# Kernel tuning notes

Measured on AMD Instinct MI355X. Metric: run time of the kernel, lower is better.

Reference implementation:

```python
import jax, jax.numpy as jnp
import numpy as np

N = 200000   # active voxels
K = 27       # 3^3 kernel offsets
C = 64       # feature channels (in == out -> residual is Identity)
EPS = 1e-5   # BatchNorm eps (torch default)


def setup_inputs() -> dict:
    key = jax.random.key(0)
    k0, k1, k2, k3 = jax.random.split(key, 4)
    x = jax.random.normal(k0, (N, C), dtype=jnp.float32)
    # neighbor map: for each output voxel and kernel offset, index of input voxel
    nbr_idx = jax.random.randint(k1, (N, K), 0, N, dtype=jnp.int64)
    W1 = jax.random.normal(k2, (K, C, C), dtype=jnp.float32) * 0.05
    W2 = jax.random.normal(k3, (K, C, C), dtype=jnp.float32) * 0.05
    gamma1 = jnp.ones((C,), jnp.float32)
    beta1 = jnp.zeros((C,), jnp.float32)
    gamma2 = jnp.ones((C,), jnp.float32)
    beta2 = jnp.zeros((C,), jnp.float32)
    return {"x": x, "nbr_idx": nbr_idx, "W1": W1, "gamma1": gamma1,
            "beta1": beta1, "W2": W2, "gamma2": gamma2, "beta2": beta2}


def batchnorm(x, gamma, beta):
    # train-mode BatchNorm1d over the voxel axis (biased variance)
    mu = x.mean(axis=0)
    var = x.var(axis=0)
    return (x - mu) * jax.lax.rsqrt(var + EPS) * gamma + beta


def sparse_conv(x, nbr_idx, W):
    # gather-GEMM-scatter sparse conv, streamed over the 27 kernel offsets
    # x: [N, Cin], nbr_idx: [N, K], W: [K, Cin, Cout]
    def body(acc, kw):
        idx, Wk = kw                      # idx: [N], Wk: [Cin, Cout]
        return acc + x[idx] @ Wk, None
    acc0 = jnp.zeros((x.shape[0], W.shape[2]), x.dtype)
    acc, _ = jax.lax.scan(body, acc0, (nbr_idx.T, W))
    return acc


def reference(x, nbr_idx, W1, gamma1, beta1, W2, gamma2, beta2):
    residual = x  # in_features == out_features -> Identity residual
    out = sparse_conv(jax.nn.relu(batchnorm(x, gamma1, beta1)), nbr_idx, W1)
    out = sparse_conv(jax.nn.relu(batchnorm(out, gamma2, beta2)), nbr_idx, W2)
    return out + residual
```

## Files before the change

kernel.cpp:

```cpp
#include <hip/hip_runtime.h>


#define KOFF 27

typedef __bf16 bf16x8 __attribute__((ext_vector_type(8)));
typedef float floatx4 __attribute__((ext_vector_type(4)));

__device__ __forceinline__ unsigned short f2bf(float x) {
    union { float f; unsigned int u; } v; v.f = x;
    unsigned int u = v.u;
    unsigned int r = u + 0x7FFFu + ((u >> 16) & 1u);
    return (unsigned short)(r >> 16);
}
__device__ __forceinline__ float bf2f(unsigned short s) {
    union { float f; unsigned int u; } v; v.u = ((unsigned int)s) << 16; return v.f;
}

__global__ void prep2(const float* __restrict__ W1, const float* __restrict__ W2,
                      unsigned short* __restrict__ W1f, unsigned short* __restrict__ W2f,
                      const float* __restrict__ x, float* __restrict__ stats,
                      int total4) {
    int b = blockIdx.x, t = threadIdx.x;
    if (b < 54) {
        __shared__ float sW[64 * 68];
        int k = b % 27;
        const float* src = (b < 27 ? W1 : W2) + k * 4096;
        unsigned short* dst = (b < 27 ? W1f : W2f) + (size_t)k * 4096;
        #pragma unroll
        for (int i = 0; i < 4; ++i) {
            int i4 = t + i * 256;
            float4 v = ((const float4*)src)[i4];
            int f = i4 * 4, r = f >> 6, c = f & 63;
            sW[r * 68 + c]     = v.x;
            sW[r * 68 + c + 1] = v.y;
            sW[r * 68 + c + 2] = v.z;
            sW[r * 68 + c + 3] = v.w;
        }
        __syncthreads();
        int fi = (t >> 5) & 7, ct = fi >> 1, ks = fi & 1;
        unsigned short o[16];
        #pragma unroll
        for (int d = 0; d < 2; ++d) {
            int lane2 = (t * 2 + d) & 63, q = lane2 >> 4, l15 = lane2 & 15;
            #pragma unroll
            for (int j = 0; j < 8; ++j) {
                int cin = ks * 32 + q * 8 + j, cout = ct * 16 + l15;
                o[d * 8 + j] = f2bf(sW[cin * 68 + cout]);
            }
        }
        ((uint4*)(dst + t * 16))[0] = *(const uint4*)(o);
        ((uint4*)(dst + t * 16))[1] = *(const uint4*)(o + 8);
        return;
    }
    __shared__ float s[128];
    if (t < 128) s[t] = 0.f;
    __syncthreads();
    int i = (b - 54) * 256 + t;
    int stride = (gridDim.x - 54) * 256;
    float a0 = 0.f, a1 = 0.f, a2 = 0.f, a3 = 0.f;
    float b0 = 0.f, b1 = 0.f, b2 = 0.f, b3 = 0.f;
    for (; i < total4; i += stride) {
        float4 v = ((const float4*)x)[i];
        a0 += v.x; b0 += v.x * v.x;
        a1 += v.y; b1 += v.y * v.y;
        a2 += v.z; b2 += v.z * v.z;
        a3 += v.w; b3 += v.w * v.w;
    }
    int c0 = (t << 2) & 63;
    atomicAdd(&s[c0],     a0); atomicAdd(&s[c0 + 1],     a1);
    atomicAdd(&s[c0 + 2], a2); atomicAdd(&s[c0 + 3],     a3);
    atomicAdd(&s[64 + c0],     b0); atomicAdd(&s[64 + c0 + 1], b1);
    atomicAdd(&s[64 + c0 + 2], b2); atomicAdd(&s[64 + c0 + 3], b3);
    __syncthreads();
    if (t < 64) { atomicAdd(&stats[t], s[t]); atomicAdd(&stats[64 + t], s[64 + t]); }
}

__global__ void bn_relu_f32(const float* __restrict__ in, const float* __restrict__ sums,
                            const float* __restrict__ gamma, const float* __restrict__ beta,
                            unsigned short* __restrict__ out, int total4, float invN) {
    __shared__ float sab[128];
    int t = threadIdx.x;
    if (t < 64) {
        float mu  = sums[t] * invN;
        float var = fmaxf(sums[64 + t] * invN - mu * mu, 0.f);
        float a   = gamma[t] * rsqrtf(var + 1e-5f);
        sab[t] = a; sab[64 + t] = beta[t] - mu * a;
    }
    __syncthreads();
    int i = blockIdx.x * blockDim.x + t;
    int stride = gridDim.x * blockDim.x;
    for (; i < total4; i += stride) {
        float4 v = ((const float4*)in)[i];
        int c0 = (i << 2) & 63;
        ushort4 o;
        o.x = f2bf(fmaxf(sab[c0]     * v.x + sab[64 + c0],     0.f));
        o.y = f2bf(fmaxf(sab[c0 + 1] * v.y + sab[64 + c0 + 1], 0.f));
        o.z = f2bf(fmaxf(sab[c0 + 2] * v.z + sab[64 + c0 + 2], 0.f));
        o.w = f2bf(fmaxf(sab[c0 + 3] * v.w + sab[64 + c0 + 3], 0.f));
        ((ushort4*)out)[i] = o;
    }
}

__global__ void bn_relu_b16(const unsigned short* __restrict__ in, const float* __restrict__ sums,
                            const float* __restrict__ gamma, const float* __restrict__ beta,
                            unsigned short* __restrict__ out, int total8, float invN) {
    __shared__ float sab[128];
    int t = threadIdx.x;
    if (t < 64) {
        float mu  = sums[t] * invN;
        float var = fmaxf(sums[64 + t] * invN - mu * mu, 0.f);
        float a   = gamma[t] * rsqrtf(var + 1e-5f);
        sab[t] = a; sab[64 + t] = beta[t] - mu * a;
    }
    __syncthreads();
    int i = blockIdx.x * blockDim.x + t;
    int stride = gridDim.x * blockDim.x;
    for (; i < total8; i += stride) {
        uint4 v = ((const uint4*)in)[i];
        int c0 = (i << 3) & 63;
        unsigned int w[4] = {v.x, v.y, v.z, v.w};
        unsigned int o[4];
        #pragma unroll
        for (int p = 0; p < 4; ++p) {
            float f0 = bf2f((unsigned short)(w[p] & 0xffff));
            float f1 = bf2f((unsigned short)(w[p] >> 16));
            int c = c0 + p * 2;
            unsigned short r0 = f2bf(fmaxf(sab[c]     * f0 + sab[64 + c],     0.f));
            unsigned short r1 = f2bf(fmaxf(sab[c + 1] * f1 + sab[64 + c + 1], 0.f));
            o[p] = (unsigned int)r0 | ((unsigned int)r1 << 16);
        }
        ((uint4*)out)[i] = make_uint4(o[0], o[1], o[2], o[3]);
    }
}

#define MFMA(a, b, c) __builtin_amdgcn_mfma_f32_16x16x32_bf16(a, b, c, 0, 0, 0)
#define WAIT_LGKM0() __builtin_amdgcn_s_waitcnt(0xC07F)

__global__ __launch_bounds__(256, 4) void spconv(
        const unsigned short* __restrict__ h,
        const int* __restrict__ idx,
        const unsigned short* __restrict__ Wf,
        unsigned short* __restrict__ outb,
        float* __restrict__ outf,
        const float* __restrict__ resid,
        float* __restrict__ stats,
        int N) {
    __shared__ float4 arena[1088];
    __shared__ float sred[128];
    unsigned short* sBb = (unsigned short*)arena;
    float* sE = (float*)arena;

    int t = threadIdx.x, lane = t & 63, wid = t >> 6;
    int q = lane >> 4, l15 = lane & 15;
    int base = blockIdx.x * 128;
    if (t < 128) sred[t] = 0.f;

    int r0 = base + wid * 32 + l15;
    int r1 = r0 + 16;
    const int* ip0 = idx + (size_t)min(r0, N - 1) * KOFF;
    const int* ip1 = idx + (size_t)min(r1, N - 1) * KOFF;
    int qo = q * 8;

    floatx4 acc[2][4];
    #pragma unroll
    for (int a_ = 0; a_ < 2; ++a_)
        #pragma unroll
        for (int b_ = 0; b_ < 4; ++b_)
            acc[a_][b_] = floatx4{0.f, 0.f, 0.f, 0.f};

    bf16x8 A0[4], A1[4], A2[4];
    {
        int g0 = ip0[0], g1 = ip1[0];
        const unsigned short* p0 = h + ((size_t)g0 << 6) + qo;
        const unsigned short* p1 = h + ((size_t)g1 << 6) + qo;
        A0[0] = *(const bf16x8*)p0; A0[1] = *(const bf16x8*)(p0 + 32);
        A0[2] = *(const bf16x8*)p1; A0[3] = *(const bf16x8*)(p1 + 32);
        g0 = ip0[1]; g1 = ip1[1];
        p0 = h + ((size_t)g0 << 6) + qo;
        p1 = h + ((size_t)g1 << 6) + qo;
        A1[0] = *(const bf16x8*)p0; A1[1] = *(const bf16x8*)(p0 + 32);
        A1[2] = *(const bf16x8*)p1; A1[3] = *(const bf16x8*)(p1 + 32);
    }
    int gc0 = ip0[2], gc1 = ip1[2];

    const uint4* Wf4 = (const uint4*)Wf;
    int so = wid * 64 + lane;
    uint4 bs0 = Wf4[so], bs1 = Wf4[256 + so];
    ((uint4*)sBb)[so] = bs0; ((uint4*)sBb)[256 + so] = bs1;
    bs0 = Wf4[512 + so]; bs1 = Wf4[512 + 256 + so];

#define COMPUTE(ACUR, CB) {                                                    \
    const bf16x8* bp = (const bf16x8*)(sBb + (CB) * 4096);                     \
    bf16x8 f0 = bp[lane], f1 = bp[64 + lane], f2 = bp[128 + lane], f3 = bp[192 + lane]; \
    acc[0][0] = MFMA(ACUR[0], f0, acc[0][0]); acc[0][0] = MFMA(ACUR[1], f1, acc[0][0]); \
    acc[0][1] = MFMA(ACUR[0], f2, acc[0][1]); acc[0][1] = MFMA(ACUR[1], f3, acc[0][1]); \
    acc[1][0] = MFMA(ACUR[2], f0, acc[1][0]); acc[1][0] = MFMA(ACUR[3], f1, acc[1][0]); \
    acc[1][1] = MFMA(ACUR[2], f2, acc[1][1]); acc[1][1] = MFMA(ACUR[3], f3, acc[1][1]); \
    f0 = bp[256 + lane]; f1 = bp[320 + lane]; f2 = bp[384 + lane]; f3 = bp[448 + lane]; \
    acc[0][2] = MFMA(ACUR[0], f0, acc[0][2]); acc[0][2] = MFMA(ACUR[1], f1, acc[0][2]); \
    acc[0][3] = MFMA(ACUR[0], f2, acc[0][3]); acc[0][3] = MFMA(ACUR[1], f3, acc[0][3]); \
    acc[1][2] = MFMA(ACUR[2], f0, acc[1][2]); acc[1][2] = MFMA(ACUR[3], f1, acc[1][2]); \
    acc[1][3] = MFMA(ACUR[2], f2, acc[1][3]); acc[1][3] = MFMA(ACUR[3], f3, acc[1][3]); \
}

#define BODY_FULL(ACUR, ALD, KRT, CB, NB) {                                    \
    WAIT_LGKM0();                                                              \
    __builtin_amdgcn_s_barrier();                                              \
    ((uint4*)sBb)[(NB) * 512 + so] = bs0;                                      \
    ((uint4*)sBb)[(NB) * 512 + 256 + so] = bs1;                                \
    bs0 = Wf4[((KRT) + 2) * 512 + so]; bs1 = Wf4[((KRT) + 2) * 512 + 256 + so];\
    {                                                                          \
        const unsigned short* p0 = h + ((size_t)gc0 << 6) + qo;                \
        const unsigned short* p1 = h + ((size_t)gc1 << 6) + qo;                \
        ALD[0] = *(const bf16x8*)p0; ALD[1] = *(const bf16x8*)(p0 + 32);       \
        ALD[2] = *(const bf16x8*)p1; ALD[3] = *(const bf16x8*)(p1 + 32);       \
    }                                                                          \
    gc0 = ip0[(KRT) + 3]; gc1 = ip1[(KRT) + 3];                                \
    COMPUTE(ACUR, CB)                                                          \
}

    #pragma unroll 1
    for (int kk = 0; kk < 24; kk += 6) {
        BODY_FULL(A0, A2, kk + 0, 0, 1)
        BODY_FULL(A1, A0, kk + 1, 1, 0)
        BODY_FULL(A2, A1, kk + 2, 0, 1)
        BODY_FULL(A0, A2, kk + 3, 1, 0)
        BODY_FULL(A1, A0, kk + 4, 0, 1)
        BODY_FULL(A2, A1, kk + 5, 1, 0)
    }
    {
        WAIT_LGKM0();
        __builtin_amdgcn_s_barrier();
        ((uint4*)sBb)[512 + so] = bs0; ((uint4*)sBb)[512 + 256 + so] = bs1;
        bs0 = Wf4[26 * 512 + so]; bs1 = Wf4[26 * 512 + 256 + so];
        {
            const unsigned short* p0 = h + ((size_t)gc0 << 6) + qo;
            const unsigned short* p1 = h + ((size_t)gc1 << 6) + qo;
            A2[0] = *(const bf16x8*)p0; A2[1] = *(const bf16x8*)(p0 + 32);
            A2[2] = *(const bf16x8*)p1; A2[3] = *(const bf16x8*)(p1 + 32);
        }
        COMPUTE(A0, 0)
    }
    {
        WAIT_LGKM0();
        __builtin_amdgcn_s_barrier();
        ((uint4*)sBb)[so] = bs0; ((uint4*)sBb)[256 + so] = bs1;
        COMPUTE(A1, 1)
    }
    {
        WAIT_LGKM0();
        __builtin_amdgcn_s_barrier();
        COMPUTE(A2, 0)
    }
#undef BODY_FULL
#undef COMPUTE

    if (stats) {
        #pragma unroll
        for (int ct = 0; ct < 4; ++ct) {
            float s1 = 0.f, s2 = 0.f;
            #pragma unroll
            for (int rt = 0; rt < 2; ++rt)
                #pragma unroll
                for (int r = 0; r < 4; ++r) {
                    int rowc = base + wid * 32 + rt * 16 + q * 4 + r;
                    float vv = (rowc < N) ? acc[rt][ct][r] : 0.f;
                    s1 += vv; s2 += vv * vv;
                }
            s1 += __shfl_xor(s1, 16); s2 += __shfl_xor(s2, 16);
            s1 += __shfl_xor(s1, 32); s2 += __shfl_xor(s2, 32);
            if (q == 0) {
                atomicAdd(&sred[ct * 16 + l15], s1);
                atomicAdd(&sred[64 + ct * 16 + l15], s2);
            }
        }
    }

    __syncthreads();

    #pragma unroll
    for (int hf = 0; hf < 2; ++hf) {
        if ((wid >> 1) == hf) {
            int lrow0 = (wid & 1) * 32;
            #pragma unroll
            for (int rt = 0; rt < 2; ++rt)
                #pragma unroll
                for (int ct = 0; ct < 4; ++ct)
                    #pragma unroll
                    for (int r = 0; r < 4; ++r)
                        sE[(lrow0 + rt * 16 + q * 4 + r) * 68 + ct * 16 + l15] = acc[rt][ct][r];
        }
        __syncthreads();
        if (hf == 0 && stats && t < 64) {
            atomicAdd(&stats[t], sred[t]);
            atomicAdd(&stats[64 + t], sred[64 + t]);
        }
        int rr = t >> 2, cc = t & 3;
        int grow = base + hf * 64 + rr;
        if (grow < N) {
            const float* sp = sE + rr * 68 + cc * 16;
            if (outb) {
                unsigned short o[16];
                #pragma unroll
                for (int j = 0; j < 16; ++j) o[j] = f2bf(sp[j]);
                unsigned short* op = outb + ((size_t)grow << 6) + cc * 16;
                ((uint4*)op)[0] = *(const uint4*)(o);
                ((uint4*)op)[1] = *(const uint4*)(o + 8);
            } else {
                const float* rp = resid + ((size_t)grow << 6) + cc * 16;
                float* op = outf + ((size_t)grow << 6) + cc * 16;
                #pragma unroll
                for (int j = 0; j < 4; ++j) {
                    float4 v = *(const float4*)(sp + j * 4);
                    float4 rv = *(const float4*)(rp + j * 4);
                    v.x += rv.x; v.y += rv.y; v.z += rv.z; v.w += rv.w;
                    *(float4*)(op + j * 4) = v;
                }
            }
        }
        if (hf == 0) __syncthreads();
    }
}

extern "C" void kernel_launch(void* const* d_in, const int* in_sizes, int n_in,
                              void* d_out, int out_size, void* d_ws, size_t ws_size,
                              hipStream_t stream) {
    const float* x      = (const float*)d_in[0];
    const int*   nbr    = (const int*)  d_in[1];
    const float* W1     = (const float*)d_in[2];
    const float* gamma1 = (const float*)d_in[3];
    const float* beta1  = (const float*)d_in[4];
    const float* W2     = (const float*)d_in[5];
    const float* gamma2 = (const float*)d_in[6];
    const float* beta2  = (const float*)d_in[7];
    float* out = (float*)d_out;

    int N = in_sizes[0] / 64;
    float invN = 1.0f / (float)N;

    char* ws = (char*)d_ws;
    float*          stats = (float*)ws;
    unsigned short* W1f   = (unsigned short*)(ws + 4096);
    unsigned short* W2f   = W1f + 110592;
    unsigned short* hbuf  = W2f + 110592;
    unsigned short* out1b = hbuf + (size_t)N * 64;

    int nb = (N + 127) / 128;

    hipMemsetAsync(stats, 0, 2048, stream);
    prep2<<<54 + 512, 256, 0, stream>>>(W1, W2, W1f, W2f, x, stats, N * 16);
    bn_relu_f32<<<768, 256, 0, stream>>>(x, stats, gamma1, beta1, hbuf, N * 16, invN);
    spconv<<<nb, 256, 0, stream>>>(hbuf, nbr, W1f, out1b, nullptr, nullptr, stats + 256, N);
    bn_relu_b16<<<768, 256, 0, stream>>>(out1b, stats + 256, gamma2, beta2, hbuf, N * 8, invN);
    spconv<<<nb, 256, 0, stream>>>(hbuf, nbr, W2f, nullptr, out, x, nullptr, N);
}
```

Before: 404.5 us.

## Fuse BN1 stats, weight prep and BN1 apply via grid-wide barrier

Merges the weight-conversion/stat-reduction kernel and the first BN+ReLU kernel into one launch. Each thread keeps its slice of x in registers (17 float4), a software grid barrier on a global counter waits for all blocks to finish the statistics, and then the normalized bf16 output is written from the registers. This removes one kernel launch and a second full read of x, at the cost of heavy register use and a grid barrier that needs all 822 blocks to be resident at once or it deadlocks.

```diff
diff --git a/kernel.cpp b/kernel.cpp
--- a/kernel.cpp
+++ b/kernel.cpp
@@ -16,25 +16,57 @@
     union { float f; unsigned int u; } v; v.u = ((unsigned int)s) << 16; return v.f;
 }
 
-__global__ void prep2(const float* __restrict__ W1, const float* __restrict__ W2,
-                      unsigned short* __restrict__ W1f, unsigned short* __restrict__ W2f,
-                      const float* __restrict__ x, float* __restrict__ stats,
-                      int total4) {
+__global__ __launch_bounds__(256, 4) void prep_bn1(
+        const float* __restrict__ W1, const float* __restrict__ W2,
+        unsigned short* __restrict__ W1f, unsigned short* __restrict__ W2f,
+        const float* __restrict__ x, float* __restrict__ stats,
+        const float* __restrict__ gamma, const float* __restrict__ beta,
+        unsigned short* __restrict__ hbuf, int total4, float invN, int nb) {
+    __shared__ float sW[64 * 68];
+    __shared__ float s[128];
     int b = blockIdx.x, t = threadIdx.x;
-    if (b < 54) {
-        __shared__ float sW[64 * 68];
-        int k = b % 27;
-        const float* src = (b < 27 ? W1 : W2) + k * 4096;
-        unsigned short* dst = (b < 27 ? W1f : W2f) + (size_t)k * 4096;
-        #pragma unroll
-        for (int i = 0; i < 4; ++i) {
-            int i4 = t + i * 256;
-            float4 v = ((const float4*)src)[i4];
+    unsigned* bar = (unsigned*)(stats + 448);
+    const int S = 768 * 256;
+
+    float4 v[17];
+    float a0 = 0.f, a1 = 0.f, a2 = 0.f, a3 = 0.f;
+    float b0 = 0.f, b1 = 0.f, b2 = 0.f, b3 = 0.f;
+    int c0 = (t << 2) & 63;
+    if (b < 768) {
+        if (t < 128) s[t] = 0.f;
+        __syncthreads();
+        int tid = b * 256 + t;
+        #pragma unroll
+        for (int j = 0; j < 17; ++j) {
+            int i = tid + j * S;
+            if (i < total4) {
+                v[j] = ((const float4*)x)[i];
+                a0 += v[j].x; b0 += v[j].x * v[j].x;
+                a1 += v[j].y; b1 += v[j].y * v[j].y;
+                a2 += v[j].z; b2 += v[j].z * v[j].z;
+                a3 += v[j].w; b3 += v[j].w * v[j].w;
+            }
+        }
+        atomicAdd(&s[c0],     a0); atomicAdd(&s[c0 + 1],     a1);
+        atomicAdd(&s[c0 + 2], a2); atomicAdd(&s[c0 + 3],     a3);
+        atomicAdd(&s[64 + c0],     b0); atomicAdd(&s[64 + c0 + 1], b1);
+        atomicAdd(&s[64 + c0 + 2], b2); atomicAdd(&s[64 + c0 + 3], b3);
+        __syncthreads();
+        if (t < 128) atomicAdd(&stats[t], s[t]);
+    } else {
+        int wb = b - 768;
+        int k = wb % 27;
+        const float* src = (wb < 27 ? W1 : W2) + k * 4096;
+        unsigned short* dst = (wb < 27 ? W1f : W2f) + (size_t)k * 4096;
+        #pragma unroll
+        for (int ii = 0; ii < 4; ++ii) {
+            int i4 = t + ii * 256;
+            float4 w = ((const float4*)src)[i4];
             int f = i4 * 4, r = f >> 6, c = f & 63;
-            sW[r * 68 + c]     = v.x;
-            sW[r * 68 + c + 1] = v.y;
-            sW[r * 68 + c + 2] = v.z;
-            sW[r * 68 + c + 3] = v.w;
+            sW[r * 68 + c]     = w.x;
+            sW[r * 68 + c + 1] = w.y;
+            sW[r * 68 + c + 2] = w.z;
+            sW[r * 68 + c + 3] = w.w;
         }
         __syncthreads();
         int fi = (t >> 5) & 7, ct = fi >> 1, ks = fi & 1;
@@ -50,54 +82,41 @@
         }
         ((uint4*)(dst + t * 16))[0] = *(const uint4*)(o);
         ((uint4*)(dst + t * 16))[1] = *(const uint4*)(o + 8);
-        return;
-    }
-    __shared__ float s[128];
-    if (t < 128) s[t] = 0.f;
-    __syncthreads();
-    int i = (b - 54) * 256 + t;
-    int stride = (gridDim.x - 54) * 256;
-    float a0 = 0.f, a1 = 0.f, a2 = 0.f, a3 = 0.f;
-    float b0 = 0.f, b1 = 0.f, b2 = 0.f, b3 = 0.f;
-    for (; i < total4; i += stride) {
-        float4 v = ((const float4*)x)[i];
-        a0 += v.x; b0 += v.x * v.x;
-        a1 += v.y; b1 += v.y * v.y;
-        a2 += v.z; b2 += v.z * v.z;
-        a3 += v.w; b3 += v.w * v.w;
-    }
-    int c0 = (t << 2) & 63;
-    atomicAdd(&s[c0],     a0); atomicAdd(&s[c0 + 1],     a1);
-    atomicAdd(&s[c0 + 2], a2); atomicAdd(&s[c0 + 3],     a3);
-    atomicAdd(&s[64 + c0],     b0); atomicAdd(&s[64 + c0 + 1], b1);
-    atomicAdd(&s[64 + c0 + 2], b2); atomicAdd(&s[64 + c0 + 3], b3);
-    __syncthreads();
-    if (t < 64) { atomicAdd(&stats[t], s[t]); atomicAdd(&stats[64 + t], s[64 + t]); }
-}
-
-__global__ void bn_relu_f32(const float* __restrict__ in, const float* __restrict__ sums,
-                            const float* __restrict__ gamma, const float* __restrict__ beta,
-                            unsigned short* __restrict__ out, int total4, float invN) {
-    __shared__ float sab[128];
-    int t = threadIdx.x;
+    }
+
+    __syncthreads();
+    if (t == 0) {
+        __hip_atomic_fetch_add(bar, 1u, __ATOMIC_ACQ_REL, __HIP_MEMORY_SCOPE_AGENT);
+        while (__hip_atomic_load(bar, __ATOMIC_ACQUIRE, __HIP_MEMORY_SCOPE_AGENT)
+               < (unsigned)nb)
+            __builtin_amdgcn_s_sleep(32);
+    }
+    __syncthreads();
+    if (b >= 768) return;
+
     if (t < 64) {
-        float mu  = sums[t] * invN;
-        float var = fmaxf(sums[64 + t] * invN - mu * mu, 0.f);
+        float s1 = __hip_atomic_load(&stats[t],      __ATOMIC_RELAXED, __HIP_MEMORY_SCOPE_AGENT);
+        float s2 = __hip_atomic_load(&stats[64 + t], __ATOMIC_RELAXED, __HIP_MEMORY_SCOPE_AGENT);
+        float mu  = s1 * invN;
+        float var = fmaxf(s2 * invN - mu * mu, 0.f);
         float a   = gamma[t] * rsqrtf(var + 1e-5f);
-        sab[t] = a; sab[64 + t] = beta[t] - mu * a;
-    }
-    __syncthreads();
-    int i = blockIdx.x * blockDim.x + t;
-    int stride = gridDim.x * blockDim.x;
-    for (; i < total4; i += stride) {
-        float4 v = ((const float4*)in)[i];
-        int c0 = (i << 2) & 63;
-        ushort4 o;
-        o.x = f2bf(fmaxf(sab[c0]     * v.x + sab[64 + c0],     0.f));
-        o.y = f2bf(fmaxf(sab[c0 + 1] * v.y + sab[64 + c0 + 1], 0.f));
-        o.z = f2bf(fmaxf(sab[c0 + 2] * v.z + sab[64 + c0 + 2], 0.f));
-        o.w = f2bf(fmaxf(sab[c0 + 3] * v.w + sab[64 + c0 + 3], 0.f));
-        ((ushort4*)out)[i] = o;
+        s[t] = a; s[64 + t] = beta[t] - mu * a;
+    }
+    __syncthreads();
+    float ca0 = s[c0],      ca1 = s[c0 + 1],      ca2 = s[c0 + 2],      ca3 = s[c0 + 3];
+    float cb0 = s[64 + c0], cb1 = s[64 + c0 + 1], cb2 = s[64 + c0 + 2], cb3 = s[64 + c0 + 3];
+    int tid = b * 256 + t;
+    #pragma unroll
+    for (int j = 0; j < 17; ++j) {
+        int i = tid + j * S;
+        if (i < total4) {
+            ushort4 o;
+            o.x = f2bf(fmaxf(ca0 * v[j].x + cb0, 0.f));
+            o.y = f2bf(fmaxf(ca1 * v[j].y + cb1, 0.f));
+            o.z = f2bf(fmaxf(ca2 * v[j].z + cb2, 0.f));
+            o.w = f2bf(fmaxf(ca3 * v[j].w + cb3, 0.f));
+            ((ushort4*)hbuf)[i] = o;
+        }
     }
 }
 
@@ -346,10 +365,12 @@
     unsigned short* out1b = hbuf + (size_t)N * 64;
 
     int nb = (N + 127) / 128;
+    int total4 = N * 16;
+    int pgrid = 822;
 
     hipMemsetAsync(stats, 0, 2048, stream);
-    prep2<<<54 + 512, 256, 0, stream>>>(W1, W2, W1f, W2f, x, stats, N * 16);
-    bn_relu_f32<<<768, 256, 0, stream>>>(x, stats, gamma1, beta1, hbuf, N * 16, invN);
+    prep_bn1<<<pgrid, 256, 0, stream>>>(W1, W2, W1f, W2f, x, stats,
+                                        gamma1, beta1, hbuf, total4, invN, pgrid);
     spconv<<<nb, 256, 0, stream>>>(hbuf, nbr, W1f, out1b, nullptr, nullptr, stats + 256, N);
     bn_relu_b16<<<768, 256, 0, stream>>>(out1b, stats + 256, gamma2, beta2, hbuf, N * 8, invN);
     spconv<<<nb, 256, 0, stream>>>(hbuf, nbr, W2f, nullptr, out, x, nullptr, N);
```

New measurement: 436.9 us. 1.08x slower.
